# Optimization experiments

Measured on AMD Instinct MI355X. Metric: run time of the kernel, lower is better.

## Reference

```python
import jax, jax.numpy as jnp
import numpy as np
from jax import lax

B, S, D, F, E, K = 4, 2048, 2048, 8192, 8, 2


def setup_inputs() -> dict:
    key = jax.random.key(0)
    ks = jax.random.split(key, 4)
    sd = 1.0 / np.sqrt(D)
    sf = 1.0 / np.sqrt(F)
    return {
        "hidden_states": jax.random.normal(ks[0], (B, S, D), dtype=jnp.float32),
        "router_w": jax.random.normal(ks[1], (D, E), dtype=jnp.float32) * sd,
        "w1": jax.random.normal(ks[2], (E, D, F), dtype=jnp.float32) * sd,
        "b1": jnp.zeros((E, F), dtype=jnp.float32),
        "w2": jax.random.normal(ks[3], (E, F, D), dtype=jnp.float32) * sf,
        "b2": jnp.zeros((E, D), dtype=jnp.float32),
        "top_k": K,
    }


def reference(hidden_states, router_w, w1, b1, w2, b2, top_k):
    b, s, d = hidden_states.shape
    x = hidden_states.reshape(-1, d)  # [T, D] flat tokens
    # Router: top-k over expert logits, softmax over the selected logits.
    logits = x @ router_w                      # [T, E]
    top_vals, top_idx = lax.top_k(logits, top_k)  # [T, K]
    scores = jax.nn.softmax(top_vals, axis=-1)    # [T, K]

    out = jnp.zeros_like(x)
    n_experts = w1.shape[0]
    for e in range(n_experts):  # fixed small expert count
        # per-token combine weight for this expert (0 if not routed)
        cw = jnp.sum(jnp.where(top_idx == e, scores, 0.0), axis=-1)  # [T]
        h = jax.nn.gelu(x @ w1[e] + b1[e], approximate=False)        # [T, F]
        out = out + cw[:, None] * (h @ w2[e] + b2[e])                # masked combine
    out = out.reshape(b, s, d)
    return out + hidden_states  # use_residual=True
```

## Files before the change

kernel.cpp:

```cpp
#include <hip/hip_runtime.h>

#define T_TOK 8192
#define DIM   2048
#define FFN   8192
#define NE    8
#define TOPK  2

typedef unsigned short ushort_t;
typedef unsigned short ushort8  __attribute__((ext_vector_type(8)));
typedef unsigned short ushort4v __attribute__((ext_vector_type(4)));
typedef short bf16x8 __attribute__((ext_vector_type(8)));
typedef float f32x4  __attribute__((ext_vector_type(4)));

__device__ __forceinline__ ushort_t f2bf(float f) {
  unsigned int u = __float_as_uint(f);
  u += 0x7FFFu + ((u >> 16) & 1u);
  return (ushort_t)(u >> 16);
}
__device__ __forceinline__ float bf2f(ushort_t u) {
  return __uint_as_float(((unsigned int)u) << 16);
}

__device__ __forceinline__ void gload16(const void* g, void* l) {
  __builtin_amdgcn_global_load_lds((const __attribute__((address_space(1))) void*)g,
                                   (__attribute__((address_space(3))) void*)l, 16, 0, 0);
}
__device__ __forceinline__ unsigned lds_off(const ushort_t* p) {
  return (unsigned)(uintptr_t)(__attribute__((address_space(3))) const ushort_t*)p;
}
__device__ __forceinline__ bf16x8 ds_read128(unsigned off) {
  bf16x8 r;
  asm volatile("ds_read_b128 %0, %1" : "=v"(r) : "v"(off));
  return r;
}

__device__ __forceinline__ float gelu_exact(float v) {
  float s = v * 0.70710678118654752f;
  float a = fabsf(s);
  float t = __builtin_amdgcn_rcpf(1.0f + 0.3275911f * a);
  float p = t * (0.254829592f +
            t * (-0.284496736f +
            t * (1.421413741f +
            t * (-1.453152027f +
            t * 1.061405429f))));
  float er = 1.0f - p * __expf(-a * a);
  er = copysignf(er, s);
  return 0.5f * v * (1.0f + er);
}

__global__ __launch_bounds__(256) void k_router(
    const float* __restrict__ x, const float* __restrict__ rw, ushort_t* __restrict__ xbf,
    int* __restrict__ tidx, float* __restrict__ twt, int* __restrict__ counts) {
  int t = blockIdx.x;
  int tid = threadIdx.x;
  int lane = tid & 63, wave = tid >> 6;
  float acc[NE];
#pragma unroll
  for (int e = 0; e < NE; e++) acc[e] = 0.f;
  const float* xr = x + (size_t)t * DIM;
  ushort_t* xbr = xbf + (size_t)t * DIM;
#pragma unroll
  for (int it = 0; it < 2; it++) {
    int d4 = it * 1024 + tid * 4;
    float4 v = *reinterpret_cast<const float4*>(xr + d4);
    ushort4v o;
    o.x = f2bf(v.x); o.y = f2bf(v.y); o.z = f2bf(v.z); o.w = f2bf(v.w);
    *reinterpret_cast<ushort4v*>(xbr + d4) = o;
    const float* r0p = rw + (size_t)d4 * NE;
    float xv[4] = {v.x, v.y, v.z, v.w};
#pragma unroll
    for (int j = 0; j < 4; j++) {
      const float* r = r0p + j * NE;
#pragma unroll
      for (int e = 0; e < NE; e++) acc[e] += xv[j] * r[e];
    }
  }
  __shared__ float wsum[4][NE];
#pragma unroll
  for (int e = 0; e < NE; e++) {
    float v = acc[e];
#pragma unroll
    for (int off = 32; off > 0; off >>= 1) v += __shfl_down(v, off);
    if (lane == 0) wsum[wave][e] = v;
  }
  __syncthreads();
  if (tid == 0) {
    float lg[NE];
#pragma unroll
    for (int e = 0; e < NE; e++) lg[e] = wsum[0][e] + wsum[1][e] + wsum[2][e] + wsum[3][e];
    int i0 = 0; float v0 = lg[0];
#pragma unroll
    for (int e = 1; e < NE; e++) if (lg[e] > v0) { v0 = lg[e]; i0 = e; }
    int i1 = -1; float v1 = -3.4e38f;
#pragma unroll
    for (int e = 0; e < NE; e++) if (e != i0 && lg[e] > v1) { v1 = lg[e]; i1 = e; }
    float e1 = expf(v1 - v0);
    float s = 1.f + e1;
    tidx[t * 2 + 0] = i0; tidx[t * 2 + 1] = i1;
    twt[t * 2 + 0] = 1.f / s; twt[t * 2 + 1] = e1 / s;
    atomicAdd(&counts[i0], 1);
    atomicAdd(&counts[i1], 1);
  }
}

#define TT 64
__global__ __launch_bounds__(256) void k_wcvt(const float* __restrict__ in,
                                              ushort_t* __restrict__ outp, int R, int C) {
  __shared__ float t[TT][TT + 1];
  int e = blockIdx.z;
  const float* src = in + (size_t)e * R * C;
  ushort_t* dst = outp + (size_t)e * R * C;
  int r0 = blockIdx.y * TT, c0 = blockIdx.x * TT;
  int tid = threadIdx.x;
  int rr = tid >> 4;
  int c4 = tid & 15;
#pragma unroll
  for (int i = 0; i < 4; i++) {
    int r = rr + i * 16;
    float4 v = *reinterpret_cast<const float4*>(src + (size_t)(r0 + r) * C + c0 + c4 * 4);
    t[r][c4 * 4 + 0] = v.x; t[r][c4 * 4 + 1] = v.y;
    t[r][c4 * 4 + 2] = v.z; t[r][c4 * 4 + 3] = v.w;
  }
  __syncthreads();
  int c = tid >> 2, rs = tid & 3;
  ushort8 v0, v1;
#pragma unroll
  for (int i = 0; i < 8; i++) {
    v0[i] = f2bf(t[rs * 16 + i][c]);
    v1[i] = f2bf(t[rs * 16 + 8 + i][c]);
  }
  ushort_t* drow = dst + (size_t)(c0 + c) * R + r0 + rs * 16;
  *reinterpret_cast<ushort8*>(drow) = v0;
  *reinterpret_cast<ushort8*>(drow + 8) = v1;
}

__global__ void k_scan(const int* __restrict__ counts, int* __restrict__ offsets) {
  if (threadIdx.x == 0) {
    int s = 0;
    for (int e = 0; e < NE; e++) { offsets[e] = s; s += counts[e]; }
    offsets[NE] = s;
  }
}

__global__ void k_fill(const int* __restrict__ tidx, const float* __restrict__ twt,
                       const int* __restrict__ offsets, int* __restrict__ cursors,
                       int* __restrict__ ltok, float* __restrict__ lwt, int* __restrict__ ppos) {
  int t = blockIdx.x * blockDim.x + threadIdx.x;
  if (t >= T_TOK) return;
#pragma unroll
  for (int k = 0; k < TOPK; k++) {
    int e = tidx[t * 2 + k];
    int pos = atomicAdd(&cursors[e], 1);
    int p = offsets[e] + pos;
    ltok[p] = t;
    lwt[p] = twt[t * 2 + k];
    ppos[t * 2 + k] = p;
  }
}

__device__ __forceinline__ void xcd_decode(int lin, int nwg, int nx, int& xt, int& yt) {
  int q = nwg >> 3;
  int w = (lin & 7) * q + (lin >> 3);
  xt = w % nx;
  yt = w / nx;
}

#define QBM 256
#define QBN 256
#define QBK 64
#define QHALF_E (128 * 64)
#define QSLOT_E (2 * QHALF_E)

#define GEMM8_PIPE(NT_)                                                                 \
  const int NT = (NT_);                                                                 \
  STA(0, 0, 0); STA(0, 1, 0);                                                           \
  STB(0, 0, 0); STB(0, 1, 0);                                                           \
  STB(1, 0, QBK); STB(1, 1, QBK);                                                       \
  asm volatile("s_waitcnt vmcnt(4)" ::: "memory");                                      \
  __builtin_amdgcn_s_barrier();                                                         \
  for (int T = 0; T < NT; ++T) {                                                        \
    int slot = T & 1;                                                                   \
    unsigned cb = (unsigned)(slot * QSLOT_E * 2);                                       \
    bf16x8 bv[4][2];                                                                    \
    _Pragma("unroll")                                                                   \
    for (int q = 0; q < 4; q++) {                                                       \
      bf16x8 af[2][2];                                                                  \
      if (q == 0) {                                                                     \
        _Pragma("unroll")                                                               \
        for (int n = 0; n < 4; n++) {                                                   \
          bv[n][0] = ds_read128(boff[n][0] + cb);                                       \
          bv[n][1] = ds_read128(boff[n][1] + cb);                                       \
        }                                                                               \
      }                                                                                 \
      _Pragma("unroll")                                                                 \
      for (int mf = 0; mf < 2; mf++) {                                                  \
        af[mf][0] = ds_read128(aoff[q * 2 + mf][0] + cb);                               \
        af[mf][1] = ds_read128(aoff[q * 2 + mf][1] + cb);                               \
      }                                                                                 \
      if (q == 0 && T + 1 < NT) STA(slot ^ 1, 0, (T + 1) * QBK);                        \
      if (q == 1) {                                                                     \
        if (T + 1 < NT) STA(slot ^ 1, 1, (T + 1) * QBK);                                \
        if (T + 2 < NT) STB(slot, 0, (T + 2) * QBK);                                    \
      }                                                                                 \
      if (q == 2 && T + 2 < NT) STB(slot, 1, (T + 2) * QBK);                            \
      __builtin_amdgcn_sched_barrier(0);                                                \
      __builtin_amdgcn_s_barrier();                                                     \
      asm volatile("s_waitcnt lgkmcnt(0)" ::: "memory");                                \
      __builtin_amdgcn_sched_barrier(0);                                                \
      __builtin_amdgcn_s_setprio(1);                                                    \
      _Pragma("unroll")                                                                 \
      for (int mf = 0; mf < 2; mf++)                                                    \
        _Pragma("unroll")                                                               \
        for (int nf = 0; nf < 4; nf++) {                                                \
          acc[q * 2 + mf][nf] = __builtin_amdgcn_mfma_f32_16x16x32_bf16(                \
              af[mf][0], bv[nf][0], acc[q * 2 + mf][nf], 0, 0, 0);                      \
          acc[q * 2 + mf][nf] = __builtin_amdgcn_mfma_f32_16x16x32_bf16(                \
              af[mf][1], bv[nf][1], acc[q * 2 + mf][nf], 0, 0, 0);                      \
        }                                                                               \
      __builtin_amdgcn_s_setprio(0);                                                    \
      __builtin_amdgcn_sched_barrier(0);                                                \
      if (q == 3) {                                                                     \
        if (T < NT - 2) { asm volatile("s_waitcnt vmcnt(4)" ::: "memory"); }            \
        else            { asm volatile("s_waitcnt vmcnt(0)" ::: "memory"); }            \
        __builtin_amdgcn_sched_barrier(0);                                              \
      }                                                                                 \
      __builtin_amdgcn_s_barrier();                                                     \
      __builtin_amdgcn_sched_barrier(0);                                                \
    }                                                                                   \
  }

#define GEMM8_SETUP()                                                                   \
  int tid = threadIdx.x;                                                                \
  int wid = tid >> 6, lane = tid & 63;                                                  \
  int wm = wid >> 2, wn = wid & 3;                                                      \
  int lm = lane & 15, lg = lane >> 4;                                                   \
  unsigned abase = lds_off(As), bbase = lds_off(Bs);                                    \
  unsigned aoff[8][2], boff[4][2];                                                      \
  _Pragma("unroll")                                                                     \
  for (int m = 0; m < 8; m++)                                                           \
    _Pragma("unroll")                                                                   \
    for (int kk = 0; kk < 2; kk++)                                                      \
      aoff[m][kk] = abase + (unsigned)((wm * QHALF_E + (m * 16 + lm) * 64 +             \
                                        (((kk * 4 + lg) ^ (lm & 7)) * 8)) * 2);         \
  _Pragma("unroll")                                                                     \
  for (int n = 0; n < 4; n++)                                                           \
    _Pragma("unroll")                                                                   \
    for (int kk = 0; kk < 2; kk++)                                                      \
      boff[n][kk] = bbase + (unsigned)(((wn >> 1) * QHALF_E +                           \
                                        ((wn & 1) * 64 + n * 16 + lm) * 64 +            \
                                        (((kk * 4 + lg) ^ (lm & 7)) * 8)) * 2);         \
  f32x4 acc[8][4];                                                                      \
  _Pragma("unroll")                                                                     \
  for (int m = 0; m < 8; m++)                                                           \
    _Pragma("unroll")                                                                   \
    for (int n = 0; n < 4; n++) acc[m][n] = (f32x4){0.f, 0.f, 0.f, 0.f};

__global__ __launch_bounds__(512) void k_gemm1(
    const ushort_t* __restrict__ xbf, const ushort_t* __restrict__ w1t, const float* __restrict__ b1,
    const int* __restrict__ counts, const int* __restrict__ offsets,
    const int* __restrict__ ltok, ushort_t* __restrict__ H) {
  int e = blockIdx.z;
  int cnt = counts[e];
  int xt, yt;
  xcd_decode(blockIdx.x, (T_TOK / QBM) * (FFN / QBN), T_TOK / QBM, xt, yt);
  int row0 = xt * QBM;
  if (row0 >= cnt) return;
  int base = offsets[e];
  int col0 = yt * QBN;
  const ushort_t* Bt = w1t + (size_t)e * DIM * FFN;

  __shared__ __align__(16) ushort_t As[2 * QSLOT_E];
  __shared__ __align__(16) ushort_t Bs[2 * QSLOT_E];

  const ushort_t* aS[2][2]; const ushort_t* bS[2][2];
#pragma unroll
  for (int l = 0; l < 2; l++) {
    int c = l * 512 + threadIdx.x;
    int rr = c >> 3;
    int s8 = (c & 7) ^ (rr & 7);
#pragma unroll
    for (int h = 0; h < 2; h++) {
      int ar = min(row0 + h * 128 + rr, cnt - 1);
      aS[h][l] = xbf + (size_t)ltok[base + ar] * DIM + s8 * 8;
      bS[h][l] = Bt + (size_t)(col0 + h * 128 + rr) * DIM + s8 * 8;
    }
  }
  int swid = threadIdx.x >> 6;
  auto STA = [&](int slot, int h, int k0) {
#pragma unroll
    for (int l = 0; l < 2; l++)
      gload16(aS[h][l] + k0, As + slot * QSLOT_E + h * QHALF_E + (l * 512 + swid * 64) * 8);
  };
  auto STB = [&](int slot, int h, int k0) {
#pragma unroll
    for (int l = 0; l < 2; l++)
      gload16(bS[h][l] + k0, Bs + slot * QSLOT_E + h * QHALF_E + (l * 512 + swid * 64) * 8);
  };

  GEMM8_SETUP();
  GEMM8_PIPE(DIM / QBK);

#pragma unroll
  for (int m = 0; m < 8; m++) {
#pragma unroll
    for (int n = 0; n < 4; n++) {
      int f = col0 + wn * 64 + n * 16 + lm;
      float bias = b1[e * FFN + f];
#pragma unroll
      for (int r = 0; r < 4; r++) {
        int row = row0 + wm * 128 + m * 16 + lg * 4 + r;
        if (row < cnt) {
          float v = acc[m][n][r] + bias;
          H[(size_t)(base + row) * FFN + f] = f2bf(gelu_exact(v));
        }
      }
    }
  }
}

__global__ __launch_bounds__(512) void k_gemm2(
    const ushort_t* __restrict__ H, const ushort_t* __restrict__ w2t, const float* __restrict__ b2,
    const int* __restrict__ counts, const int* __restrict__ offsets,
    const float* __restrict__ lwt, ushort_t* __restrict__ contrib) {
  int e = blockIdx.z;
  int cnt = counts[e];
  int xt, yt;
  xcd_decode(blockIdx.x, (T_TOK / QBM) * (DIM / QBN), T_TOK / QBM, xt, yt);
  int row0 = xt * QBM;
  if (row0 >= cnt) return;
  int base = offsets[e];
  int col0 = yt * QBN;
  const ushort_t* Bt = w2t + (size_t)e * DIM * FFN;

  __shared__ __align__(16) ushort_t As[2 * QSLOT_E];
  __shared__ __align__(16) ushort_t Bs[2 * QSLOT_E];

  const ushort_t* aS[2][2]; const ushort_t* bS[2][2];
#pragma unroll
  for (int l = 0; l < 2; l++) {
    int c = l * 512 + threadIdx.x;
    int rr = c >> 3;
    int s8 = (c & 7) ^ (rr & 7);
#pragma unroll
    for (int h = 0; h < 2; h++) {
      int ar = min(row0 + h * 128 + rr, cnt - 1);
      aS[h][l] = H + (size_t)(base + ar) * FFN + s8 * 8;
      bS[h][l] = Bt + (size_t)(col0 + h * 128 + rr) * FFN + s8 * 8;
    }
  }
  int swid = threadIdx.x >> 6;
  auto STA = [&](int slot, int h, int k0) {
#pragma unroll
    for (int l = 0; l < 2; l++)
      gload16(aS[h][l] + k0, As + slot * QSLOT_E + h * QHALF_E + (l * 512 + swid * 64) * 8);
  };
  auto STB = [&](int slot, int h, int k0) {
#pragma unroll
    for (int l = 0; l < 2; l++)
      gload16(bS[h][l] + k0, Bs + slot * QSLOT_E + h * QHALF_E + (l * 512 + swid * 64) * 8);
  };

  GEMM8_SETUP();
  GEMM8_PIPE(FFN / QBK);

#pragma unroll
  for (int m = 0; m < 8; m++) {
#pragma unroll
    for (int n = 0; n < 4; n++) {
      int d = col0 + wn * 64 + n * 16 + lm;
      float bias = b2[e * DIM + d];
#pragma unroll
      for (int r = 0; r < 4; r++) {
        int row = row0 + wm * 128 + m * 16 + lg * 4 + r;
        if (row < cnt) {
          float v = (acc[m][n][r] + bias) * lwt[base + row];
          contrib[(size_t)(base + row) * DIM + d] = f2bf(v);
        }
      }
    }
  }
}

__global__ void k_combine(const float* __restrict__ x, const ushort_t* __restrict__ contrib,
                          const int* __restrict__ ppos, float* __restrict__ out) {
  int i = blockIdx.x * blockDim.x + threadIdx.x;
  int t = i / (DIM / 4);
  int dq = i % (DIM / 4);
  int p0 = ppos[t * 2 + 0], p1 = ppos[t * 2 + 1];
  float4 xv = reinterpret_cast<const float4*>(x)[i];
  ushort4v c0 = reinterpret_cast<const ushort4v*>(contrib + (size_t)p0 * DIM)[dq];
  ushort4v c1 = reinterpret_cast<const ushort4v*>(contrib + (size_t)p1 * DIM)[dq];
  float4 o;
  o.x = xv.x + bf2f(c0.x) + bf2f(c1.x);
  o.y = xv.y + bf2f(c0.y) + bf2f(c1.y);
  o.z = xv.z + bf2f(c0.z) + bf2f(c1.z);
  o.w = xv.w + bf2f(c0.w) + bf2f(c1.w);
  reinterpret_cast<float4*>(out)[i] = o;
}

extern "C" void kernel_launch(void* const* d_in, const int* in_sizes, int n_in,
                              void* d_out, int out_size, void* d_ws, size_t ws_size,
                              hipStream_t stream) {
  const float* x  = (const float*)d_in[0];
  const float* rw = (const float*)d_in[1];
  const float* w1 = (const float*)d_in[2];
  const float* b1 = (const float*)d_in[3];
  const float* w2 = (const float*)d_in[4];
  const float* b2 = (const float*)d_in[5];
  float* out = (float*)d_out;
  char* ws = (char*)d_ws;

  const size_t MB = 1u << 20;
  int*   counts  = (int*)(ws);
  int*   offsets = (int*)(ws + 64);
  int*   cursors = (int*)(ws + 128);
  int*   tidx    = (int*)(ws + 1 * MB);
  float* twt     = (float*)(ws + 2 * MB);
  int*   ltok    = (int*)(ws + 3 * MB);
  float* lwt     = (float*)(ws + 4 * MB);
  int*   ppos    = (int*)(ws + 5 * MB);
  ushort_t* xbf     = (ushort_t*)(ws + 8 * MB);
  ushort_t* contrib = (ushort_t*)(ws + 8 * MB);
  ushort_t* Hbuf    = (ushort_t*)(ws + 72 * MB);
  ushort_t* w1t     = (ushort_t*)(ws + 328 * MB);
  ushort_t* w2t     = (ushort_t*)(ws + 328 * MB);
  const size_t NEED = 584 * MB;
  if (ws_size < NEED) {
    hipMemsetAsync(d_out, 0, (size_t)out_size * sizeof(float), stream);
    return;
  }

  hipMemsetAsync(ws, 0, 256, stream);
  k_router<<<T_TOK, 256, 0, stream>>>(x, rw, xbf, tidx, twt, counts);
  k_scan<<<1, 64, 0, stream>>>(counts, offsets);
  k_fill<<<T_TOK / 256, 256, 0, stream>>>(tidx, twt, offsets, cursors, ltok, lwt, ppos);
  k_wcvt<<<dim3(FFN / TT, DIM / TT, NE), 256, 0, stream>>>(w1, w1t, DIM, FFN);
  k_gemm1<<<dim3((T_TOK / QBM) * (FFN / QBN), 1, NE), 512, 0, stream>>>(xbf, w1t, b1, counts, offsets, ltok, Hbuf);
  k_wcvt<<<dim3(DIM / TT, FFN / TT, NE), 256, 0, stream>>>(w2, w2t, FFN, DIM);
  k_gemm2<<<dim3((T_TOK / QBM) * (DIM / QBN), 1, NE), 512, 0, stream>>>(Hbuf, w2t, b2, counts, offsets, lwt, contrib);
  k_combine<<<dim3((T_TOK * (size_t)DIM / 4) / 256), 256, 0, stream>>>(x, contrib, ppos, out);
}
```

Before: 2.000 ms.

## Software-pipeline LDS A-fragment reads with MFMA and cut per-phase barriers

```diff
diff --git a/kernel.cpp b/kernel.cpp
--- a/kernel.cpp
+++ b/kernel.cpp
@@ -171,62 +171,79 @@
 #define QHALF_E (128 * 64)
 #define QSLOT_E (2 * QHALF_E)
 
+#define RD_A(RR, qq)                                                                    \
+  RR[0][0] = ds_read128(aoff[(qq) * 2 + 0][0] + cb);                                    \
+  RR[0][1] = ds_read128(aoff[(qq) * 2 + 0][1] + cb);                                    \
+  RR[1][0] = ds_read128(aoff[(qq) * 2 + 1][0] + cb);                                    \
+  RR[1][1] = ds_read128(aoff[(qq) * 2 + 1][1] + cb);
+
+#define PH_MFMA(qq, RR)                                                                 \
+  __builtin_amdgcn_s_setprio(1);                                                        \
+  _Pragma("unroll")                                                                     \
+  for (int mf = 0; mf < 2; mf++)                                                        \
+    _Pragma("unroll")                                                                   \
+    for (int nf = 0; nf < 4; nf++) {                                                    \
+      acc[(qq) * 2 + mf][nf] = __builtin_amdgcn_mfma_f32_16x16x32_bf16(                 \
+          RR[mf][0], bv[nf][0], acc[(qq) * 2 + mf][nf], 0, 0, 0);                       \
+      acc[(qq) * 2 + mf][nf] = __builtin_amdgcn_mfma_f32_16x16x32_bf16(                 \
+          RR[mf][1], bv[nf][1], acc[(qq) * 2 + mf][nf], 0, 0, 0);                       \
+    }                                                                                   \
+  __builtin_amdgcn_s_setprio(0);
+
 #define GEMM8_PIPE(NT_)                                                                 \
   const int NT = (NT_);                                                                 \
   STA(0, 0, 0); STA(0, 1, 0);                                                           \
   STB(0, 0, 0); STB(0, 1, 0);                                                           \
   STB(1, 0, QBK); STB(1, 1, QBK);                                                       \
   asm volatile("s_waitcnt vmcnt(4)" ::: "memory");                                      \
-  __builtin_amdgcn_s_barrier();                                                         \
   for (int T = 0; T < NT; ++T) {                                                        \
     int slot = T & 1;                                                                   \
     unsigned cb = (unsigned)(slot * QSLOT_E * 2);                                       \
-    bf16x8 bv[4][2];                                                                    \
+    bf16x8 bv[4][2], rA[2][2], rB[2][2];                                                \
+                                                                                \
+    __builtin_amdgcn_sched_barrier(0);                                                  \
+    __builtin_amdgcn_s_barrier();                                                       \
+    __builtin_amdgcn_sched_barrier(0);                                                  \
     _Pragma("unroll")                                                                   \
-    for (int q = 0; q < 4; q++) {                                                       \
-      bf16x8 af[2][2];                                                                  \
-      if (q == 0) {                                                                     \
-        _Pragma("unroll")                                                               \
-        for (int n = 0; n < 4; n++) {                                                   \
-          bv[n][0] = ds_read128(boff[n][0] + cb);                                       \
-          bv[n][1] = ds_read128(boff[n][1] + cb);                                       \
-        }                                                                               \
-      }                                                                                 \
-      _Pragma("unroll")                                                                 \
-      for (int mf = 0; mf < 2; mf++) {                                                  \
-        af[mf][0] = ds_read128(aoff[q * 2 + mf][0] + cb);                               \
-        af[mf][1] = ds_read128(aoff[q * 2 + mf][1] + cb);                               \
-      }                                                                                 \
-      if (q == 0 && T + 1 < NT) STA(slot ^ 1, 0, (T + 1) * QBK);                        \
-      if (q == 1) {                                                                     \
-        if (T + 1 < NT) STA(slot ^ 1, 1, (T + 1) * QBK);                                \
-        if (T + 2 < NT) STB(slot, 0, (T + 2) * QBK);                                    \
-      }                                                                                 \
-      if (q == 2 && T + 2 < NT) STB(slot, 1, (T + 2) * QBK);                            \
-      __builtin_amdgcn_sched_barrier(0);                                                \
-      __builtin_amdgcn_s_barrier();                                                     \
-      asm volatile("s_waitcnt lgkmcnt(0)" ::: "memory");                                \
-      __builtin_amdgcn_sched_barrier(0);                                                \
-      __builtin_amdgcn_s_setprio(1);                                                    \
-      _Pragma("unroll")                                                                 \
-      for (int mf = 0; mf < 2; mf++)                                                    \
-        _Pragma("unroll")                                                               \
-        for (int nf = 0; nf < 4; nf++) {                                                \
-          acc[q * 2 + mf][nf] = __builtin_amdgcn_mfma_f32_16x16x32_bf16(                \
-              af[mf][0], bv[nf][0], acc[q * 2 + mf][nf], 0, 0, 0);                      \
-          acc[q * 2 + mf][nf] = __builtin_amdgcn_mfma_f32_16x16x32_bf16(                \
-              af[mf][1], bv[nf][1], acc[q * 2 + mf][nf], 0, 0, 0);                      \
-        }                                                                               \
-      __builtin_amdgcn_s_setprio(0);                                                    \
-      __builtin_amdgcn_sched_barrier(0);                                                \
-      if (q == 3) {                                                                     \
-        if (T < NT - 2) { asm volatile("s_waitcnt vmcnt(4)" ::: "memory"); }            \
-        else            { asm volatile("s_waitcnt vmcnt(0)" ::: "memory"); }            \
-        __builtin_amdgcn_sched_barrier(0);                                              \
-      }                                                                                 \
-      __builtin_amdgcn_s_barrier();                                                     \
-      __builtin_amdgcn_sched_barrier(0);                                                \
+    for (int n = 0; n < 4; n++) {                                                       \
+      bv[n][0] = ds_read128(boff[n][0] + cb);                                           \
+      bv[n][1] = ds_read128(boff[n][1] + cb);                                           \
     }                                                                                   \
+    RD_A(rA, 0)                                                                         \
+    RD_A(rB, 1)                                                                         \
+    if (T + 1 < NT) { STA(slot ^ 1, 0, (T + 1) * QBK); }                                \
+    __builtin_amdgcn_sched_barrier(0);                                                  \
+    asm volatile("s_waitcnt lgkmcnt(4)" ::: "memory");                                  \
+    __builtin_amdgcn_sched_barrier(0);                                                  \
+    PH_MFMA(0, rA)                                                                      \
+                                                                                \
+    __builtin_amdgcn_sched_barrier(0);                                                  \
+    __builtin_amdgcn_s_barrier();                                                       \
+    __builtin_amdgcn_sched_barrier(0);                                                  \
+    RD_A(rA, 2)                                                                         \
+    if (T + 1 < NT) { STA(slot ^ 1, 1, (T + 1) * QBK); }                                \
+    if (T + 2 < NT) { STB(slot, 0, (T + 2) * QBK); }                                    \
+    __builtin_amdgcn_sched_barrier(0);                                                  \
+    asm volatile("s_waitcnt lgkmcnt(4)" ::: "memory");                                  \
+    __builtin_amdgcn_sched_barrier(0);                                                  \
+    PH_MFMA(1, rB)                                                                      \
+                               \
+    __builtin_amdgcn_sched_barrier(0);                                                  \
+    RD_A(rB, 3)                                                                         \
+    if (T + 2 < NT) { STB(slot, 1, (T + 2) * QBK); }                                    \
+    __builtin_amdgcn_sched_barrier(0);                                                  \
+    asm volatile("s_waitcnt lgkmcnt(4)" ::: "memory");                                  \
+    __builtin_amdgcn_sched_barrier(0);                                                  \
+    PH_MFMA(2, rA)                                                                      \
+                                                               \
+    __builtin_amdgcn_sched_barrier(0);                                                  \
+    asm volatile("s_waitcnt lgkmcnt(0)" ::: "memory");                                  \
+    __builtin_amdgcn_sched_barrier(0);                                                  \
+    PH_MFMA(3, rB)                                                                      \
+    __builtin_amdgcn_sched_barrier(0);                                                  \
+    if (T < NT - 2) { asm volatile("s_waitcnt vmcnt(4)" ::: "memory"); }                \
+    else            { asm volatile("s_waitcnt vmcnt(0)" ::: "memory"); }                \
+    __builtin_amdgcn_sched_barrier(0);                                                  \
   }
 
 #define GEMM8_SETUP()                                                                   \
```

New measurement: 1.892 ms, median of 2. -5.4%, faster.
